# Kernel optimization log

Measured on AMD Instinct MI355X. Metric: run time of the kernel, lower is better.

## Reference

```python
import jax, jax.numpy as jnp
import numpy as np

D = 4096  # in_features == out_features (required: LayerNorm(in_features) applied to out-dim output)
B, S = 4, 4096
LN_EPS = 1e-5


def setup_inputs() -> dict:
    key = jax.random.key(0)
    ks = jax.random.split(key, 5)
    return {
        "x": jax.random.normal(ks[0], (B, S, D), dtype=jnp.float32),
        "weight": jax.random.normal(ks[1], (D, D), dtype=jnp.float32),  # [out, in]
        "bias": jax.random.normal(ks[2], (D,), dtype=jnp.float32),
        "g": jax.random.normal(ks[3], (D,), dtype=jnp.float32),   # input scale [in]
        "h": jax.random.normal(ks[4], (D,), dtype=jnp.float32),   # output scale [out]
        "ln_gamma": jnp.ones((D,), dtype=jnp.float32),
        "ln_beta": jnp.zeros((D,), dtype=jnp.float32),
    }


def reference(x, weight, bias, g, h, ln_gamma, ln_beta):
    sign_w = jnp.sign(weight)                      # binarized weight [out, in]
    xg = x * g                                     # per-input-channel scale
    y = jnp.einsum("bsi,oi->bso", xg, sign_w) + bias
    y = y * h                                      # per-output-channel scale
    mu = jnp.mean(y, axis=-1, keepdims=True)
    var = jnp.mean(jnp.square(y - mu), axis=-1, keepdims=True)
    out = (y - mu) * jax.lax.rsqrt(var + LN_EPS) * ln_gamma + ln_beta
    return out
```

## Files before the change

kernel.cpp:

```cpp
#include <hip/hip_runtime.h>
#include <hip/hip_bf16.h>
#include <stdint.h>

typedef __bf16 bf16x8 __attribute__((ext_vector_type(8)));
typedef float f32x4 __attribute__((ext_vector_type(4)));

#define GLDS16(gp, lp) __builtin_amdgcn_global_load_lds( \
    (const __attribute__((address_space(1))) unsigned int*)(gp), \
    (__attribute__((address_space(3))) unsigned int*)(lp), 16, 0, 0)

#define BARRIER() asm volatile("s_barrier" ::: "memory")
#define VMCNT(n)  asm volatile("s_waitcnt vmcnt(" #n ")" ::: "memory")


__global__ __launch_bounds__(256) void prep_xg(
    const float* __restrict__ x, const float* __restrict__ g,
    __bf16* __restrict__ out, long total, int K)
{
    long i = ((long)blockIdx.x * blockDim.x + threadIdx.x) * 8;
    const long stride = (long)gridDim.x * blockDim.x * 8;
    for (; i < total; i += stride) {
        const int k = (int)(i & (long)(K - 1));
        f32x4 x0 = *(const f32x4*)(x + i);
        f32x4 x1 = *(const f32x4*)(x + i + 4);
        f32x4 g0 = *(const f32x4*)(g + k);
        f32x4 g1 = *(const f32x4*)(g + k + 4);
        bf16x8 o;
        #pragma unroll
        for (int j = 0; j < 4; ++j) o[j]     = (__bf16)(x0[j] * g0[j]);
        #pragma unroll
        for (int j = 0; j < 4; ++j) o[4 + j] = (__bf16)(x1[j] * g1[j]);
        *(bf16x8*)(out + i) = o;
    }
}

__global__ __launch_bounds__(256) void prep_sign(
    const float* __restrict__ w, __bf16* __restrict__ out, long total)
{
    long i = ((long)blockIdx.x * blockDim.x + threadIdx.x) * 8;
    const long stride = (long)gridDim.x * blockDim.x * 8;
    for (; i < total; i += stride) {
        f32x4 w0 = *(const f32x4*)(w + i);
        f32x4 w1 = *(const f32x4*)(w + i + 4);
        bf16x8 o;
        #pragma unroll
        for (int j = 0; j < 4; ++j)
            o[j]     = (__bf16)((w0[j] > 0.f) ? 1.f : ((w0[j] < 0.f) ? -1.f : 0.f));
        #pragma unroll
        for (int j = 0; j < 4; ++j)
            o[4 + j] = (__bf16)((w1[j] > 0.f) ? 1.f : ((w1[j] < 0.f) ? -1.f : 0.f));
        *(bf16x8*)(out + i) = o;
    }
}


template<bool BF16OUT>
__global__ __launch_bounds__(512, 2) void gemm_8p(
    const __bf16* __restrict__ A, const __bf16* __restrict__ B,
    const float* __restrict__ bias, const float* __restrict__ h,
    __bf16* __restrict__ yb, float* __restrict__ yf, int M, int N, int K)
{
    extern __shared__ __bf16 sm[];

    const int xcd = blockIdx.x & 7;
    const int l = blockIdx.x >> 3;
    const int bn = xcd * 2 + (l & 1);
    const int bm = l >> 1;

    const int t = threadIdx.x;
    const int lane = t & 63;
    const int w = t >> 6;
    const int wm = w >> 2;
    const int wn = w & 3;
    const int sl = lane >> 4;
    const int fr = lane & 15;

    const int ra8 = (wm * 16 + fr) * 8;
    const int rb8 = (wn * 16 + fr) * 8;
    const int stA = w * 2048 + lane * 8;
    const int stB = 16384 + stA;

    const __bf16* gA = A + (long)(bm * 256 + lane) * K + w * 8;
    const __bf16* gB = B + (long)(bn * 256 + lane) * K + w * 8;

    const int NT = K / 64;
    const long K64 = (long)K * 64;
    const long K128 = (long)K * 128;

#define STG_A(c, T, half) do { \
    GLDS16(gA + (long)(half) * K128 + (long)(T) * 64,             &sm[(c) * 32768 + stA + (half) * 1024]); \
    GLDS16(gA + (long)(half) * K128 + K64 + (long)(T) * 64,       &sm[(c) * 32768 + stA + (half) * 1024 + 512]); \
} while (0)
#define STG_B(c, T, half) do { \
    GLDS16(gB + (long)(half) * K128 + (long)(T) * 64,             &sm[(c) * 32768 + stB + (half) * 1024]); \
    GLDS16(gB + (long)(half) * K128 + K64 + (long)(T) * 64,       &sm[(c) * 32768 + stB + (half) * 1024 + 512]); \
} while (0)

#define RD_A(dst, cb, m, kk)  dst = *(bf16x8*)&sm[(cb) + ((kk) * 4 + sl) * 2048 + (m) * 256 + ra8]
#define RD_B(dst, cb, n, kk)  dst = *(bf16x8*)&sm[(cb) + 16384 + ((kk) * 4 + sl) * 2048 + (n) * 512 + rb8]
#define MF(d, a, b) d = __builtin_amdgcn_mfma_f32_16x16x32_bf16(a, b, d, 0, 0, 0)

    f32x4 acc[8][4] = {};
    bf16x8 aF[4][2], aH[4][2], b0F[2][2], b1F[2][2];

    STG_A(0, 0, 0); STG_B(0, 0, 0); STG_B(0, 0, 1); STG_A(0, 0, 1);
    STG_A(1, 1, 0); STG_B(1, 1, 0); STG_B(1, 1, 1);
    VMCNT(6);
    BARRIER();

    for (int i = 0; i < NT / 2; ++i) {
        const int t1 = 2 * i + 1;
        const int nx0 = 2 * i + 2;
        const int nx1 = 2 * i + 3;
        const bool more = (nx0 < NT);

        #pragma unroll
        for (int kk = 0; kk < 2; ++kk) {
            #pragma unroll
            for (int m = 0; m < 4; ++m) RD_A(aF[m][kk], 0, m, kk);
            #pragma unroll
            for (int n = 0; n < 2; ++n) RD_B(b0F[n][kk], 0, n, kk);
            #pragma unroll
            for (int n = 0; n < 2; ++n) RD_B(b1F[n][kk], 0, n + 2, kk);
        }
        STG_A(1, t1, 1);
        __builtin_amdgcn_s_setprio(1);
        #pragma unroll
        for (int kk = 0; kk < 2; ++kk)
            #pragma unroll
            for (int m = 0; m < 4; ++m)
                #pragma unroll
                for (int n = 0; n < 2; ++n) MF(acc[m][n], aF[m][kk], b0F[n][kk]);
        __builtin_amdgcn_s_setprio(0);
        BARRIER();

        #pragma unroll
        for (int kk = 0; kk < 2; ++kk)
            #pragma unroll
            for (int m = 0; m < 4; ++m) RD_A(aH[m][kk], 0, m + 4, kk);
        if (more) STG_A(0, nx0, 0);
        __builtin_amdgcn_s_setprio(1);
        #pragma unroll
        for (int kk = 0; kk < 2; ++kk)
            #pragma unroll
            for (int m = 0; m < 4; ++m)
                #pragma unroll
                for (int n = 0; n < 2; ++n) MF(acc[m][n + 2], aF[m][kk], b1F[n][kk]);
        __builtin_amdgcn_s_setprio(0);
        BARRIER();

        if (more) STG_B(0, nx0, 0);
        __builtin_amdgcn_s_setprio(1);
        #pragma unroll
        for (int kk = 0; kk < 2; ++kk)
            #pragma unroll
            for (int m = 0; m < 4; ++m)
                #pragma unroll
                for (int n = 0; n < 2; ++n) MF(acc[m + 4][n + 2], aH[m][kk], b1F[n][kk]);
        __builtin_amdgcn_s_setprio(0);
        BARRIER();

        if (more) { STG_B(0, nx0, 1); VMCNT(6); } else { VMCNT(0); }
        __builtin_amdgcn_s_setprio(1);
        #pragma unroll
        for (int kk = 0; kk < 2; ++kk)
            #pragma unroll
            for (int m = 0; m < 4; ++m)
                #pragma unroll
                for (int n = 0; n < 2; ++n) MF(acc[m + 4][n], aH[m][kk], b0F[n][kk]);
        __builtin_amdgcn_s_setprio(0);
        BARRIER();

        #pragma unroll
        for (int kk = 0; kk < 2; ++kk) {
            #pragma unroll
            for (int m = 0; m < 4; ++m) RD_A(aF[m][kk], 32768, m, kk);
            #pragma unroll
            for (int n = 0; n < 2; ++n) RD_B(b0F[n][kk], 32768, n, kk);
            #pragma unroll
            for (int n = 0; n < 2; ++n) RD_B(b1F[n][kk], 32768, n + 2, kk);
        }
        if (more) STG_A(0, nx0, 1);
        __builtin_amdgcn_s_setprio(1);
        #pragma unroll
        for (int kk = 0; kk < 2; ++kk)
            #pragma unroll
            for (int m = 0; m < 4; ++m)
                #pragma unroll
                for (int n = 0; n < 2; ++n) MF(acc[m][n], aF[m][kk], b0F[n][kk]);
        __builtin_amdgcn_s_setprio(0);
        BARRIER();

        #pragma unroll
        for (int kk = 0; kk < 2; ++kk)
            #pragma unroll
            for (int m = 0; m < 4; ++m) RD_A(aH[m][kk], 32768, m + 4, kk);
        if (more) STG_A(1, nx1, 0);
        __builtin_amdgcn_s_setprio(1);
        #pragma unroll
        for (int kk = 0; kk < 2; ++kk)
            #pragma unroll
            for (int m = 0; m < 4; ++m)
                #pragma unroll
                for (int n = 0; n < 2; ++n) MF(acc[m][n + 2], aF[m][kk], b1F[n][kk]);
        __builtin_amdgcn_s_setprio(0);
        BARRIER();

        if (more) STG_B(1, nx1, 0);
        __builtin_amdgcn_s_setprio(1);
        #pragma unroll
        for (int kk = 0; kk < 2; ++kk)
            #pragma unroll
            for (int m = 0; m < 4; ++m)
                #pragma unroll
                for (int n = 0; n < 2; ++n) MF(acc[m + 4][n + 2], aH[m][kk], b1F[n][kk]);
        __builtin_amdgcn_s_setprio(0);
        BARRIER();

        if (more) { STG_B(1, nx1, 1); VMCNT(6); } else { VMCNT(0); }
        __builtin_amdgcn_s_setprio(1);
        #pragma unroll
        for (int kk = 0; kk < 2; ++kk)
            #pragma unroll
            for (int m = 0; m < 4; ++m)
                #pragma unroll
                for (int n = 0; n < 2; ++n) MF(acc[m + 4][n], aH[m][kk], b0F[n][kk]);
        __builtin_amdgcn_s_setprio(0);
        BARRIER();
    }

    const int cr = (lane >> 4) * 4;
    const int cc = lane & 15;
    #pragma unroll
    for (int n = 0; n < 4; ++n) {
        const int col = bn * 256 + n * 64 + wn * 16 + cc;
        const float bc = bias[col];
        const float hc = h[col];
        #pragma unroll
        for (int m = 0; m < 8; ++m) {
            const long rowb = (long)bm * 256 + m * 32 + wm * 16 + cr;
            #pragma unroll
            for (int j = 0; j < 4; ++j) {
                const float v = (acc[m][n][j] + bc) * hc;
                if (BF16OUT) {
                    union { __bf16 b; unsigned short u; } cv;
                    cv.b = (__bf16)v;
                    __builtin_nontemporal_store(cv.u,
                        (unsigned short*)yb + (rowb + j) * (long)N + col);
                } else {
                    __builtin_nontemporal_store(v, yf + (rowb + j) * (long)N + col);
                }
            }
        }
    }
#undef STG_A
#undef STG_B
#undef RD_A
#undef RD_B
#undef MF
}


__global__ __launch_bounds__(256) void ln_ws(
    const __bf16* __restrict__ ybuf, float* __restrict__ out,
    const float* __restrict__ gamma, const float* __restrict__ beta)
{
    const long r0 = (long)blockIdx.x * 2;
    const int t = threadIdx.x;
    const int lane = t & 63, wave = t >> 6;

    bf16x8 a0 = *(const bf16x8*)(ybuf + r0 * 4096 + t * 16);
    bf16x8 a1 = *(const bf16x8*)(ybuf + r0 * 4096 + t * 16 + 8);
    bf16x8 b0 = *(const bf16x8*)(ybuf + (r0 + 1) * 4096 + t * 16);
    bf16x8 b1 = *(const bf16x8*)(ybuf + (r0 + 1) * 4096 + t * 16 + 8);

    float v0[16], v1[16];
    float s0 = 0.f, q0 = 0.f, s1 = 0.f, q1 = 0.f;
    #pragma unroll
    for (int j = 0; j < 8; ++j) {
        v0[j] = (float)a0[j]; v0[8 + j] = (float)a1[j];
        v1[j] = (float)b0[j]; v1[8 + j] = (float)b1[j];
    }
    #pragma unroll
    for (int j = 0; j < 16; ++j) {
        s0 += v0[j]; q0 += v0[j] * v0[j];
        s1 += v1[j]; q1 += v1[j] * v1[j];
    }
    #pragma unroll
    for (int off = 32; off > 0; off >>= 1) {
        s0 += __shfl_down(s0, off); q0 += __shfl_down(q0, off);
        s1 += __shfl_down(s1, off); q1 += __shfl_down(q1, off);
    }
    __shared__ float red[4][4];
    if (lane == 0) { red[wave][0] = s0; red[wave][1] = q0; red[wave][2] = s1; red[wave][3] = q1; }
    __syncthreads();
    const float ts0 = red[0][0] + red[1][0] + red[2][0] + red[3][0];
    const float tq0 = red[0][1] + red[1][1] + red[2][1] + red[3][1];
    const float ts1 = red[0][2] + red[1][2] + red[2][2] + red[3][2];
    const float tq1 = red[0][3] + red[1][3] + red[2][3] + red[3][3];
    const float mu0 = ts0 * (1.0f / 4096.0f);
    const float mu1 = ts1 * (1.0f / 4096.0f);
    const float rs0 = rsqrtf(tq0 * (1.0f / 4096.0f) - mu0 * mu0 + 1e-5f);
    const float rs1 = rsqrtf(tq1 * (1.0f / 4096.0f) - mu1 * mu1 + 1e-5f);

    #pragma unroll
    for (int c = 0; c < 4; ++c) {
        f32x4 gv = *(const f32x4*)(gamma + t * 16 + c * 4);
        f32x4 bv = *(const f32x4*)(beta + t * 16 + c * 4);
        f32x4 o0, o1;
        #pragma unroll
        for (int j = 0; j < 4; ++j) {
            o0[j] = (v0[c * 4 + j] - mu0) * rs0 * gv[j] + bv[j];
            o1[j] = (v1[c * 4 + j] - mu1) * rs1 * gv[j] + bv[j];
        }
        *(f32x4*)(out + r0 * 4096 + t * 16 + c * 4) = o0;
        *(f32x4*)(out + (r0 + 1) * 4096 + t * 16 + c * 4) = o1;
    }
}


__global__ __launch_bounds__(256) void ln_inplace(
    float* __restrict__ y, const float* __restrict__ gamma,
    const float* __restrict__ beta, int N)
{
    const long row = blockIdx.x;
    float* p = y + row * (long)N;
    const int t = threadIdx.x;

    f32x4 v[4];
    float sum = 0.f, sq = 0.f;
    #pragma unroll
    for (int i = 0; i < 4; ++i) {
        v[i] = *(const f32x4*)(p + i * 1024 + t * 4);
        #pragma unroll
        for (int j = 0; j < 4; ++j) { sum += v[i][j]; sq += v[i][j] * v[i][j]; }
    }
    #pragma unroll
    for (int off = 32; off > 0; off >>= 1) {
        sum += __shfl_down(sum, off);
        sq  += __shfl_down(sq, off);
    }
    __shared__ float s1[4], s2[4];
    const int lane = t & 63, wave = t >> 6;
    if (lane == 0) { s1[wave] = sum; s2[wave] = sq; }
    __syncthreads();
    const float tot = s1[0] + s1[1] + s1[2] + s1[3];
    const float tsq = s2[0] + s2[1] + s2[2] + s2[3];
    const float mean = tot / (float)N;
    const float var = tsq / (float)N - mean * mean;
    const float rstd = rsqrtf(var + 1e-5f);

    #pragma unroll
    for (int i = 0; i < 4; ++i) {
        f32x4 ga = *(const f32x4*)(gamma + i * 1024 + t * 4);
        f32x4 be = *(const f32x4*)(beta + i * 1024 + t * 4);
        f32x4 o;
        #pragma unroll
        for (int j = 0; j < 4; ++j) o[j] = (v[i][j] - mean) * rstd * ga[j] + be[j];
        *(f32x4*)(p + i * 1024 + t * 4) = o;
    }
}


#define BMf 128
#define BNf 128
#define BKf 32
#define LDPf 40

__global__ __launch_bounds__(256) void binlin_gemm_fb(
    const float* __restrict__ x, const float* __restrict__ w,
    const float* __restrict__ bias, const float* __restrict__ g,
    const float* __restrict__ h, float* __restrict__ y,
    int M, int N, int K)
{
    __shared__ __bf16 As[BMf][LDPf];
    __shared__ __bf16 Bs[BNf][LDPf];
    const int nbn = N / BNf;
    const int bm = blockIdx.x / nbn;
    const int bn = blockIdx.x % nbn;
    const int t = threadIdx.x;
    const int lane = t & 63;
    const int wave = t >> 6;
    const int wm = wave >> 1, wn = wave & 1;
    const int row2 = t >> 2, kq = (t & 3) * 8;
    const long xbase = (long)bm * BMf * K;
    const long wbase = (long)bn * BNf * K;
    f32x4 acc[4][4] = {};
    const int fr = lane & 15;
    const int ko = (lane >> 4) * 8;
    for (int k0 = 0; k0 < K; k0 += BKf) {
        f32x4 ga = *(const f32x4*)(g + k0 + kq);
        f32x4 gb = *(const f32x4*)(g + k0 + kq + 4);
        #pragma unroll
        for (int p = 0; p < 2; ++p) {
            const int r = p * 64 + row2;
            const float* xp = x + xbase + (long)r * K + k0 + kq;
            f32x4 x0 = *(const f32x4*)xp;
            f32x4 x1 = *(const f32x4*)(xp + 4);
            bf16x8 av;
            #pragma unroll
            for (int i = 0; i < 4; ++i) av[i]     = (__bf16)(x0[i] * ga[i]);
            #pragma unroll
            for (int i = 0; i < 4; ++i) av[4 + i] = (__bf16)(x1[i] * gb[i]);
            *(bf16x8*)&As[r][kq] = av;
            const float* wp = w + wbase + (long)r * K + k0 + kq;
            f32x4 w0 = *(const f32x4*)wp;
            f32x4 w1 = *(const f32x4*)(wp + 4);
            bf16x8 bv;
            #pragma unroll
            for (int i = 0; i < 4; ++i)
                bv[i]     = (__bf16)((w0[i] > 0.f) ? 1.f : ((w0[i] < 0.f) ? -1.f : 0.f));
            #pragma unroll
            for (int i = 0; i < 4; ++i)
                bv[4 + i] = (__bf16)((w1[i] > 0.f) ? 1.f : ((w1[i] < 0.f) ? -1.f : 0.f));
            *(bf16x8*)&Bs[r][kq] = bv;
        }
        __syncthreads();
        bf16x8 af[4], bfr[4];
        #pragma unroll
        for (int m = 0; m < 4; ++m) af[m]  = *(bf16x8*)&As[wm * 64 + m * 16 + fr][ko];
        #pragma unroll
        for (int n = 0; n < 4; ++n) bfr[n] = *(bf16x8*)&Bs[wn * 64 + n * 16 + fr][ko];
        #pragma unroll
        for (int m = 0; m < 4; ++m)
            #pragma unroll
            for (int n = 0; n < 4; ++n)
                acc[m][n] = __builtin_amdgcn_mfma_f32_16x16x32_bf16(af[m], bfr[n], acc[m][n], 0, 0, 0);
        __syncthreads();
    }
    const int cr = (lane >> 4) * 4;
    const int cc = lane & 15;
    #pragma unroll
    for (int n = 0; n < 4; ++n) {
        const int col = bn * BNf + wn * 64 + n * 16 + cc;
        const float bc = bias[col];
        const float hc = h[col];
        #pragma unroll
        for (int m = 0; m < 4; ++m) {
            const long rowb = (long)bm * BMf + wm * 64 + m * 16 + cr;
            #pragma unroll
            for (int j = 0; j < 4; ++j)
                y[(rowb + j) * N + col] = (acc[m][n][j] + bc) * hc;
        }
    }
}

extern "C" void kernel_launch(void* const* d_in, const int* in_sizes, int n_in,
                              void* d_out, int out_size, void* d_ws, size_t ws_size,
                              hipStream_t stream)
{
    (void)n_in; (void)out_size;
    const float* x     = (const float*)d_in[0];
    const float* w     = (const float*)d_in[1];
    const float* bias  = (const float*)d_in[2];
    const float* g     = (const float*)d_in[3];
    const float* h     = (const float*)d_in[4];
    const float* gamma = (const float*)d_in[5];
    const float* beta  = (const float*)d_in[6];
    float* out = (float*)d_out;

    const int D = in_sizes[2];
    const long M = (long)in_sizes[0] / D;

    const size_t needA = (size_t)M * D * sizeof(__bf16);
    const size_t needB = (size_t)D * D * sizeof(__bf16);
    const size_t needY = (size_t)M * D * sizeof(__bf16);

    const bool okShape = (D == 4096 && (M % 512) == 0);

    if (okShape && ws_size >= needA + needB) {
        __bf16* xg   = (__bf16*)d_ws;
        __bf16* wsgn = (__bf16*)((char*)d_ws + needA);
        prep_xg  <<<dim3(2048), dim3(256), 0, stream>>>(x, g, xg, M * (long)D, D);
        prep_sign<<<dim3(2048), dim3(256), 0, stream>>>(w, wsgn, (long)D * D);
        dim3 grid((unsigned)((M / 256) * (D / 256)));

        if (ws_size >= needA + needB + needY) {
            __bf16* ybf = (__bf16*)((char*)d_ws + needA + needB);
            hipFuncSetAttribute((const void*)gemm_8p<true>,
                                hipFuncAttributeMaxDynamicSharedMemorySize, 131072);
            gemm_8p<true><<<grid, dim3(512), 131072, stream>>>(
                xg, wsgn, bias, h, ybf, nullptr, (int)M, D, D);
            ln_ws<<<dim3((unsigned)(M / 2)), dim3(256), 0, stream>>>(ybf, out, gamma, beta);
        } else {
            hipFuncSetAttribute((const void*)gemm_8p<false>,
                                hipFuncAttributeMaxDynamicSharedMemorySize, 131072);
            gemm_8p<false><<<grid, dim3(512), 131072, stream>>>(
                xg, wsgn, bias, h, nullptr, out, (int)M, D, D);
            ln_inplace<<<dim3((unsigned)M), dim3(256), 0, stream>>>(out, gamma, beta, D);
        }
    } else {
        dim3 grid((unsigned)((M / BMf) * (D / BNf)));
        binlin_gemm_fb<<<grid, dim3(256), 0, stream>>>(x, w, bias, g, h, out, (int)M, D, D);
        ln_inplace<<<dim3((unsigned)M), dim3(256), 0, stream>>>(out, gamma, beta, D);
    }
}
```

Before: 770.0 us.

## Pre-swizzle A into MFMA fragment layout and load it directly from global

The prep kernel now writes x*g in a tiled layout that matches the per-wave MFMA A-fragment order. The GEMM loads A fragments straight from global memory into registers instead of staging them through LDS, so only B is staged, and the shared memory request drops to 64KB. The pipeline becomes a simple per-K-tile double buffer with a single barrier per tile instead of the previous multi-phase schedule. The cost is that each wave in a row now loads A from global/L2 separately, which raises global traffic, and global latency is exposed to the MFMA stream.

```diff
diff --git a/kernel.cpp b/kernel.cpp
--- a/kernel.cpp
+++ b/kernel.cpp
@@ -13,14 +13,15 @@
 #define VMCNT(n)  asm volatile("s_waitcnt vmcnt(" #n ")" ::: "memory")
 
 
-__global__ __launch_bounds__(256) void prep_xg(
+__global__ __launch_bounds__(256) void prep_xg_t(
     const float* __restrict__ x, const float* __restrict__ g,
-    __bf16* __restrict__ out, long total, int K)
+    __bf16* __restrict__ out, long total)
 {
     long i = ((long)blockIdx.x * blockDim.x + threadIdx.x) * 8;
     const long stride = (long)gridDim.x * blockDim.x * 8;
     for (; i < total; i += stride) {
-        const int k = (int)(i & (long)(K - 1));
+        const long row = i >> 12;
+        const int k = (int)i & 4095;
         f32x4 x0 = *(const f32x4*)(x + i);
         f32x4 x1 = *(const f32x4*)(x + i + 4);
         f32x4 g0 = *(const f32x4*)(g + k);
@@ -30,7 +31,13 @@
         for (int j = 0; j < 4; ++j) o[j]     = (__bf16)(x0[j] * g0[j]);
         #pragma unroll
         for (int j = 0; j < 4; ++j) o[4 + j] = (__bf16)(x1[j] * g1[j]);
-        *(bf16x8*)(out + i) = o;
+        const long bmI = row >> 8;
+        const int r16 = (int)((row >> 4) & 15);
+        const int fr  = (int)(row & 15);
+        const int T = k >> 6;
+        const int s = (k & 63) >> 3;
+        const long oidx = ((bmI * 64 + T) * 16 + r16) * 1024 + s * 128 + fr * 8;
+        *(bf16x8*)(out + oidx) = o;
     }
 }
 
@@ -55,12 +62,13 @@
 
 
 template<bool BF16OUT>
-__global__ __launch_bounds__(512, 2) void gemm_8p(
-    const __bf16* __restrict__ A, const __bf16* __restrict__ B,
+__global__ __launch_bounds__(512, 2) void gemm_ad(
+    const __bf16* __restrict__ A,
+    const __bf16* __restrict__ B,
     const float* __restrict__ bias, const float* __restrict__ h,
     __bf16* __restrict__ yb, float* __restrict__ yf, int M, int N, int K)
 {
-    extern __shared__ __bf16 sm[];
+    extern __shared__ __bf16 smB[];
 
     const int xcd = blockIdx.x & 7;
     const int l = blockIdx.x >> 3;
@@ -75,55 +83,55 @@
     const int sl = lane >> 4;
     const int fr = lane & 15;
 
-    const int ra8 = (wm * 16 + fr) * 8;
     const int rb8 = (wn * 16 + fr) * 8;
-    const int stA = w * 2048 + lane * 8;
-    const int stB = 16384 + stA;
-
-    const __bf16* gA = A + (long)(bm * 256 + lane) * K + w * 8;
-    const __bf16* gB = B + (long)(bn * 256 + lane) * K + w * 8;
+    const int stB = w * 2048 + lane * 8;
+
+    const __bf16* gB  = B + (long)(bn * 256 + lane) * K + w * 8;
+    const __bf16* gAt = A + (long)bm * 256 * K + wm * 1024 + lane * 8;
 
     const int NT = K / 64;
     const long K64 = (long)K * 64;
     const long K128 = (long)K * 128;
 
-#define STG_A(c, T, half) do { \
-    GLDS16(gA + (long)(half) * K128 + (long)(T) * 64,             &sm[(c) * 32768 + stA + (half) * 1024]); \
-    GLDS16(gA + (long)(half) * K128 + K64 + (long)(T) * 64,       &sm[(c) * 32768 + stA + (half) * 1024 + 512]); \
+#define STG_B(c, T, half) do { \
+    GLDS16(gB + (long)(half) * K128 + (long)(T) * 64,       &smB[(c) * 16384 + stB + (half) * 1024]); \
+    GLDS16(gB + (long)(half) * K128 + K64 + (long)(T) * 64, &smB[(c) * 16384 + stB + (half) * 1024 + 512]); \
 } while (0)
-#define STG_B(c, T, half) do { \
-    GLDS16(gB + (long)(half) * K128 + (long)(T) * 64,             &sm[(c) * 32768 + stB + (half) * 1024]); \
-    GLDS16(gB + (long)(half) * K128 + K64 + (long)(T) * 64,       &sm[(c) * 32768 + stB + (half) * 1024 + 512]); \
-} while (0)
-
-#define RD_A(dst, cb, m, kk)  dst = *(bf16x8*)&sm[(cb) + ((kk) * 4 + sl) * 2048 + (m) * 256 + ra8]
-#define RD_B(dst, cb, n, kk)  dst = *(bf16x8*)&sm[(cb) + 16384 + ((kk) * 4 + sl) * 2048 + (n) * 512 + rb8]
+#define RD_B(dst, c, n, kk)  dst = *(bf16x8*)&smB[(c) * 16384 + ((kk) * 4 + sl) * 2048 + (n) * 512 + rb8]
+#define LD_AF(m, kk, T)  aF[m][kk] = *(const bf16x8*)(gAt + (long)(T) * 16384 + (m) * 2048 + (kk) * 512)
+#define LD_AH(m, kk, T)  aH[m][kk] = *(const bf16x8*)(gAt + (long)(T) * 16384 + 8192 + (m) * 2048 + (kk) * 512)
 #define MF(d, a, b) d = __builtin_amdgcn_mfma_f32_16x16x32_bf16(a, b, d, 0, 0, 0)
 
     f32x4 acc[8][4] = {};
     bf16x8 aF[4][2], aH[4][2], b0F[2][2], b1F[2][2];
 
-    STG_A(0, 0, 0); STG_B(0, 0, 0); STG_B(0, 0, 1); STG_A(0, 0, 1);
-    STG_A(1, 1, 0); STG_B(1, 1, 0); STG_B(1, 1, 1);
-    VMCNT(6);
-    BARRIER();
-
-    for (int i = 0; i < NT / 2; ++i) {
-        const int t1 = 2 * i + 1;
-        const int nx0 = 2 * i + 2;
-        const int nx1 = 2 * i + 3;
-        const bool more = (nx0 < NT);
+    STG_B(0, 0, 0); STG_B(0, 0, 1);
+    #pragma unroll
+    for (int m = 0; m < 4; ++m)
+        #pragma unroll
+        for (int kk = 0; kk < 2; ++kk) LD_AF(m, kk, 0);
+    #pragma unroll
+    for (int m = 0; m < 4; ++m)
+        #pragma unroll
+        for (int kk = 0; kk < 2; ++kk) LD_AH(m, kk, 0);
+
+    for (int ti = 0; ti < NT; ++ti) {
+        const int buf = ti & 1;
+        const bool more = (ti + 1 < NT);
+
+        VMCNT(16);
+        BARRIER();
+
+        if (more) { STG_B(buf ^ 1, ti + 1, 0); STG_B(buf ^ 1, ti + 1, 1); }
 
         #pragma unroll
         for (int kk = 0; kk < 2; ++kk) {
             #pragma unroll
-            for (int m = 0; m < 4; ++m) RD_A(aF[m][kk], 0, m, kk);
-            #pragma unroll
-            for (int n = 0; n < 2; ++n) RD_B(b0F[n][kk], 0, n, kk);
-            #pragma unroll
-            for (int n = 0; n < 2; ++n) RD_B(b1F[n][kk], 0, n + 2, kk);
-        }
-        STG_A(1, t1, 1);
+            for (int n = 0; n < 2; ++n) RD_B(b0F[n][kk], buf, n, kk);
+            #pragma unroll
+            for (int n = 0; n < 2; ++n) RD_B(b1F[n][kk], buf, n + 2, kk);
+        }
+
         __builtin_amdgcn_s_setprio(1);
         #pragma unroll
         for (int kk = 0; kk < 2; ++kk)
@@ -131,15 +139,6 @@
             for (int m = 0; m < 4; ++m)
                 #pragma unroll
                 for (int n = 0; n < 2; ++n) MF(acc[m][n], aF[m][kk], b0F[n][kk]);
-        __builtin_amdgcn_s_setprio(0);
-        BARRIER();
-
-        #pragma unroll
-        for (int kk = 0; kk < 2; ++kk)
-            #pragma unroll
-            for (int m = 0; m < 4; ++m) RD_A(aH[m][kk], 0, m + 4, kk);
-        if (more) STG_A(0, nx0, 0);
-        __builtin_amdgcn_s_setprio(1);
         #pragma unroll
         for (int kk = 0; kk < 2; ++kk)
             #pragma unroll
@@ -147,9 +146,14 @@
                 #pragma unroll
                 for (int n = 0; n < 2; ++n) MF(acc[m][n + 2], aF[m][kk], b1F[n][kk]);
         __builtin_amdgcn_s_setprio(0);
-        BARRIER();
-
-        if (more) STG_B(0, nx0, 0);
+
+        if (more) {
+            #pragma unroll
+            for (int m = 0; m < 4; ++m)
+                #pragma unroll
+                for (int kk = 0; kk < 2; ++kk) LD_AF(m, kk, ti + 1);
+        }
+
         __builtin_amdgcn_s_setprio(1);
         #pragma unroll
         for (int kk = 0; kk < 2; ++kk)
@@ -157,11 +161,6 @@
             for (int m = 0; m < 4; ++m)
                 #pragma unroll
                 for (int n = 0; n < 2; ++n) MF(acc[m + 4][n + 2], aH[m][kk], b1F[n][kk]);
-        __builtin_amdgcn_s_setprio(0);
-        BARRIER();
-
-        if (more) { STG_B(0, nx0, 1); VMCNT(6); } else { VMCNT(0); }
-        __builtin_amdgcn_s_setprio(1);
         #pragma unroll
         for (int kk = 0; kk < 2; ++kk)
             #pragma unroll
@@ -169,64 +168,13 @@
                 #pragma unroll
                 for (int n = 0; n < 2; ++n) MF(acc[m + 4][n], aH[m][kk], b0F[n][kk]);
         __builtin_amdgcn_s_setprio(0);
-        BARRIER();
-
-        #pragma unroll
-        for (int kk = 0; kk < 2; ++kk) {
-            #pragma unroll
-            for (int m = 0; m < 4; ++m) RD_A(aF[m][kk], 32768, m, kk);
-            #pragma unroll
-            for (int n = 0; n < 2; ++n) RD_B(b0F[n][kk], 32768, n, kk);
-            #pragma unroll
-            for (int n = 0; n < 2; ++n) RD_B(b1F[n][kk], 32768, n + 2, kk);
-        }
-        if (more) STG_A(0, nx0, 1);
-        __builtin_amdgcn_s_setprio(1);
-        #pragma unroll
-        for (int kk = 0; kk < 2; ++kk)
-            #pragma unroll
-            for (int m = 0; m < 4; ++m)
-                #pragma unroll
-                for (int n = 0; n < 2; ++n) MF(acc[m][n], aF[m][kk], b0F[n][kk]);
-        __builtin_amdgcn_s_setprio(0);
-        BARRIER();
-
-        #pragma unroll
-        for (int kk = 0; kk < 2; ++kk)
-            #pragma unroll
-            for (int m = 0; m < 4; ++m) RD_A(aH[m][kk], 32768, m + 4, kk);
-        if (more) STG_A(1, nx1, 0);
-        __builtin_amdgcn_s_setprio(1);
-        #pragma unroll
-        for (int kk = 0; kk < 2; ++kk)
-            #pragma unroll
-            for (int m = 0; m < 4; ++m)
-                #pragma unroll
-                for (int n = 0; n < 2; ++n) MF(acc[m][n + 2], aF[m][kk], b1F[n][kk]);
-        __builtin_amdgcn_s_setprio(0);
-        BARRIER();
-
-        if (more) STG_B(1, nx1, 0);
-        __builtin_amdgcn_s_setprio(1);
-        #pragma unroll
-        for (int kk = 0; kk < 2; ++kk)
-            #pragma unroll
-            for (int m = 0; m < 4; ++m)
-                #pragma unroll
-                for (int n = 0; n < 2; ++n) MF(acc[m + 4][n + 2], aH[m][kk], b1F[n][kk]);
-        __builtin_amdgcn_s_setprio(0);
-        BARRIER();
-
-        if (more) { STG_B(1, nx1, 1); VMCNT(6); } else { VMCNT(0); }
-        __builtin_amdgcn_s_setprio(1);
-        #pragma unroll
-        for (int kk = 0; kk < 2; ++kk)
-            #pragma unroll
-            for (int m = 0; m < 4; ++m)
-                #pragma unroll
-                for (int n = 0; n < 2; ++n) MF(acc[m + 4][n], aH[m][kk], b0F[n][kk]);
-        __builtin_amdgcn_s_setprio(0);
-        BARRIER();
+
+        if (more) {
+            #pragma unroll
+            for (int m = 0; m < 4; ++m)
+                #pragma unroll
+                for (int kk = 0; kk < 2; ++kk) LD_AH(m, kk, ti + 1);
+        }
     }
 
     const int cr = (lane >> 4) * 4;
@@ -253,10 +201,10 @@
             }
         }
     }
-#undef STG_A
 #undef STG_B
-#undef RD_A
 #undef RD_B
+#undef LD_AF
+#undef LD_AH
 #undef MF
 }
 
@@ -471,21 +419,21 @@
     if (okShape && ws_size >= needA + needB) {
         __bf16* xg   = (__bf16*)d_ws;
         __bf16* wsgn = (__bf16*)((char*)d_ws + needA);
-        prep_xg  <<<dim3(2048), dim3(256), 0, stream>>>(x, g, xg, M * (long)D, D);
+        prep_xg_t<<<dim3(2048), dim3(256), 0, stream>>>(x, g, xg, M * (long)D);
         prep_sign<<<dim3(2048), dim3(256), 0, stream>>>(w, wsgn, (long)D * D);
         dim3 grid((unsigned)((M / 256) * (D / 256)));
 
         if (ws_size >= needA + needB + needY) {
             __bf16* ybf = (__bf16*)((char*)d_ws + needA + needB);
-            hipFuncSetAttribute((const void*)gemm_8p<true>,
-                                hipFuncAttributeMaxDynamicSharedMemorySize, 131072);
-            gemm_8p<true><<<grid, dim3(512), 131072, stream>>>(
+            hipFuncSetAttribute((const void*)gemm_ad<true>,
+                                hipFuncAttributeMaxDynamicSharedMemorySize, 65536);
+            gemm_ad<true><<<grid, dim3(512), 65536, stream>>>(
                 xg, wsgn, bias, h, ybf, nullptr, (int)M, D, D);
             ln_ws<<<dim3((unsigned)(M / 2)), dim3(256), 0, stream>>>(ybf, out, gamma, beta);
         } else {
-            hipFuncSetAttribute((const void*)gemm_8p<false>,
-                                hipFuncAttributeMaxDynamicSharedMemorySize, 131072);
-            gemm_8p<false><<<grid, dim3(512), 131072, stream>>>(
+            hipFuncSetAttribute((const void*)gemm_ad<false>,
+                                hipFuncAttributeMaxDynamicSharedMemorySize, 65536);
+            gemm_ad<false><<<grid, dim3(512), 65536, stream>>>(
                 xg, wsgn, bias, h, nullptr, out, (int)M, D, D);
             ln_inplace<<<dim3((unsigned)M), dim3(256), 0, stream>>>(out, gamma, beta, D);
         }
```

Result: slower. 928.9 us (+20.6%).
